# Kernel optimization log

Hardware: AMD Instinct MI355X
Metric: run time of the kernel (lower is better)

## Reference

```python
import jax, jax.numpy as jnp
import numpy as np

B, S, DIM, H = 2, 2048, 1024, 16
DK = DIM // H  # 64
NEG = -10000000000.0


def setup_inputs() -> dict:
    key = jax.random.key(0)
    k1, k2, k3, k4, k5, k6 = jax.random.split(key, 6)
    dec_xs = jax.random.normal(k1, (B, S, DIM), dtype=jnp.float32)
    enc_xs = jax.random.normal(k2, (B, S, DIM), dtype=jnp.float32)
    mask = jax.random.randint(k3, (B, S, S), 0, 2, dtype=jnp.int32)
    # torch Linear weights: out = x @ W.T, bias=False
    sc = 1.0 / np.sqrt(DIM)
    Wq = jax.random.normal(k4, (DIM, DIM), dtype=jnp.float32) * sc
    Wkv = jax.random.normal(k5, (2 * DIM, DIM), dtype=jnp.float32) * sc
    Wo = jax.random.normal(k6, (DIM, DIM), dtype=jnp.float32) * sc
    return {"dec_xs": dec_xs, "enc_xs": enc_xs, "Wq": Wq, "Wkv": Wkv, "Wo": Wo, "mask": mask}


def reference(dec_xs, enc_xs, Wq, Wkv, Wo, mask):
    b, s, dim = enc_xs.shape
    qs = dec_xs @ Wq.T                      # [b,s,dim]  (dropout inactive in eval)
    kv = enc_xs @ Wkv.T                     # [b,s,2*dim]
    ks, vs = jnp.split(kv, 2, axis=-1)
    # head layout: view(b, s, dk, h) -- heads LAST, as in the original
    qs = qs.reshape(b, s, DK, H)
    ks = ks.reshape(b, s, DK, H)
    vs = vs.reshape(b, s, DK, H)
    scores = jnp.einsum('bqdh,bkdh->bqkh', qs, ks) / np.sqrt(DK)
    scores = jnp.where(mask[..., None] == 0, NEG, scores)
    weights = jax.nn.softmax(scores, axis=-2)  # softmax over key axis
    out = jnp.einsum('bqkh,bkdh->bqdh', weights, vs).reshape(b, s, dim)
    return out @ Wo.T
```

## Files before the change

### kernel.cpp

```cpp
#include <hip/hip_runtime.h>
#include <hip/hip_bf16.h>

#define BB 2
#define SS 2048
#define DIMM 1024
#define HH 16
#define DKK 64
#define QSCALE 0.18033688011112042592f

using bf16 = __hip_bfloat16;
typedef __attribute__((ext_vector_type(8))) short v8s;
typedef __attribute__((ext_vector_type(4))) short v4s;
typedef __attribute__((ext_vector_type(4))) float f32x4;

__device__ __forceinline__ void cvt4(const float* __restrict__ s,
                                     bf16* __restrict__ d, int idx) {
  const float4 f = ((const float4*)s)[idx];
  bf16 t[4] = {__float2bfloat16(f.x), __float2bfloat16(f.y),
               __float2bfloat16(f.z), __float2bfloat16(f.w)};
  *(v4s*)(d + (size_t)idx * 4) = *(const v4s*)t;
}

__global__ __launch_bounds__(256) void convert_pack_kernel(
    const float* __restrict__ enc, const float* __restrict__ Wkv,
    const float* __restrict__ Wo, const int* __restrict__ mask,
    bf16* __restrict__ encb, bf16* __restrict__ Wkvb, bf16* __restrict__ Wob,
    unsigned long long* __restrict__ mp) {
  const int gid = blockIdx.x * 256 + threadIdx.x;
  const int NT = 256 * 1024;
#pragma unroll
  for (int i = 0; i < 4; ++i) cvt4(enc, encb, gid + i * NT);
#pragma unroll
  for (int i = 0; i < 2; ++i) cvt4(Wkv, Wkvb, gid + i * NT);
  cvt4(Wo, Wob, gid);
  const int lane = threadIdx.x & 63;
  const int wave_id = gid >> 6;
  for (int i = 0; i < 32; ++i) {
    const size_t w = (size_t)wave_id * 32 + i;
    const unsigned long long bm = __ballot(mask[w * 64 + lane] != 0);
    if (lane == 0) mp[w] = bm;
  }
}

template <bool ISQ>
__device__ __forceinline__ void proj_body(
    int t, int m0, int h0, bool isV, const float* __restrict__ dec,
    const bf16* __restrict__ encb, const float* __restrict__ Wq,
    const bf16* __restrict__ Wkvb, bf16 (*__restrict__ As)[72],
    bf16 (*__restrict__ Bs)[72], f32x4 (&acc)[4][2], int wm, int wn, int quad,
    int l15) {
  const int sr = t >> 2;
  const int sc = (t & 3) * 16;
  const int worig = (isV ? DIMM : 0) + sr * 16 + h0;

  float4 aqf[8], bqf[4];
  v8s akb[4], bkb[2];

  auto loadA = [&](int kc) {
    if (ISQ) {
#pragma unroll
      for (int rr = 0; rr < 2; ++rr) {
        const float* p = dec + (size_t)(m0 + sr + rr * 64) * DIMM + kc + sc;
#pragma unroll
        for (int i = 0; i < 4; ++i) aqf[rr * 4 + i] = ((const float4*)p)[i];
      }
    } else {
#pragma unroll
      for (int rr = 0; rr < 2; ++rr) {
        const bf16* p = encb + (size_t)(m0 + sr + rr * 64) * DIMM + kc + sc;
#pragma unroll
        for (int i = 0; i < 2; ++i) akb[rr * 2 + i] = ((const v8s*)p)[i];
      }
    }
  };
  auto loadB = [&](int kc) {
    if (ISQ) {
      const float* p = Wq + (size_t)worig * DIMM + kc + sc;
#pragma unroll
      for (int i = 0; i < 4; ++i) bqf[i] = ((const float4*)p)[i];
    } else {
      const bf16* p = Wkvb + (size_t)worig * DIMM + kc + sc;
#pragma unroll
      for (int i = 0; i < 2; ++i) bkb[i] = ((const v8s*)p)[i];
    }
  };

  loadA(0);
  loadB(0);

  for (int kc = 0; kc < DIMM; kc += 64) {
    __syncthreads();
    if (ISQ) {
#pragma unroll
      for (int rr = 0; rr < 2; ++rr) {
        bf16 tmp[16];
#pragma unroll
        for (int i = 0; i < 4; ++i) {
          const float4 f = aqf[rr * 4 + i];
          tmp[i * 4 + 0] = __float2bfloat16(f.x);
          tmp[i * 4 + 1] = __float2bfloat16(f.y);
          tmp[i * 4 + 2] = __float2bfloat16(f.z);
          tmp[i * 4 + 3] = __float2bfloat16(f.w);
        }
        *(v8s*)&As[sr + rr * 64][sc] = *(const v8s*)&tmp[0];
        *(v8s*)&As[sr + rr * 64][sc + 8] = *(const v8s*)&tmp[8];
      }
      bf16 tb[16];
#pragma unroll
      for (int i = 0; i < 4; ++i) {
        const float4 f = bqf[i];
        tb[i * 4 + 0] = __float2bfloat16(f.x);
        tb[i * 4 + 1] = __float2bfloat16(f.y);
        tb[i * 4 + 2] = __float2bfloat16(f.z);
        tb[i * 4 + 3] = __float2bfloat16(f.w);
      }
      *(v8s*)&Bs[sr][sc] = *(const v8s*)&tb[0];
      *(v8s*)&Bs[sr][sc + 8] = *(const v8s*)&tb[8];
    } else {
#pragma unroll
      for (int rr = 0; rr < 2; ++rr) {
        *(v8s*)&As[sr + rr * 64][sc] = akb[rr * 2 + 0];
        *(v8s*)&As[sr + rr * 64][sc + 8] = akb[rr * 2 + 1];
      }
      *(v8s*)&Bs[sr][sc] = bkb[0];
      *(v8s*)&Bs[sr][sc + 8] = bkb[1];
    }
    if (kc + 64 < DIMM) {
      loadA(kc + 64);
      loadB(kc + 64);
    }
    __syncthreads();
#pragma unroll
    for (int ks = 0; ks < 2; ++ks) {
      v8s af[4], bfr[2];
#pragma unroll
      for (int i = 0; i < 4; ++i)
        af[i] = *(const v8s*)&As[wm + i * 16 + l15][ks * 32 + quad * 8];
#pragma unroll
      for (int j = 0; j < 2; ++j)
        bfr[j] = *(const v8s*)&Bs[wn + j * 16 + l15][ks * 32 + quad * 8];
#pragma unroll
      for (int i = 0; i < 4; ++i)
#pragma unroll
        for (int j = 0; j < 2; ++j)
          acc[i][j] = __builtin_amdgcn_mfma_f32_16x16x32_bf16(
              af[i], bfr[j], acc[i][j], 0, 0, 0);
    }
  }
}

__global__ __launch_bounds__(256) void proj_gemm_kernel(
    const float* __restrict__ dec, const bf16* __restrict__ encb,
    const float* __restrict__ Wq, const bf16* __restrict__ Wkvb,
    bf16* __restrict__ Qr, bf16* __restrict__ Kr, bf16* __restrict__ Vt) {
  __shared__ __align__(16) bf16 As[128][72];
  __shared__ __align__(16) bf16 Bs[64][72];
  const int t = threadIdx.x;
  const int wave = t >> 6, lane = t & 63;
  const int quad = lane >> 4, l15 = lane & 15;
  const int wm = (wave >> 1) * 64, wn = (wave & 1) * 32;
  const int bx = blockIdx.x;
  const int m0 = blockIdx.y * 128;
  const bool isQ = bx < 16;
  const int kvx = bx - 16;
  const int h0 = isQ ? bx : (kvx & 15);
  const bool isV = !isQ && (kvx >= 16);

  f32x4 acc[4][2] = {};
  if (isQ)
    proj_body<true>(t, m0, h0, false, dec, encb, Wq, Wkvb, As, Bs, acc, wm, wn,
                    quad, l15);
  else
    proj_body<false>(t, m0, h0, isV, dec, encb, Wq, Wkvb, As, Bs, acc, wm, wn,
                     quad, l15);

#pragma unroll
  for (int i = 0; i < 4; ++i) {
#pragma unroll
    for (int r = 0; r < 4; ++r) {
      const int m = m0 + wm + i * 16 + quad * 4 + r;
#pragma unroll
      for (int j = 0; j < 2; ++j) {
        const int d = wn + j * 16 + l15;
        const float v = acc[i][j][r];
        if (isQ) {
          Qr[(size_t)m * DIMM + h0 * 64 + d] = __float2bfloat16(v * QSCALE);
        } else if (!isV) {
          Kr[(size_t)m * DIMM + h0 * 64 + d] = __float2bfloat16(v);
        } else {
          const int b = m >> 11, s = m & (SS - 1);
          Vt[(((size_t)b * HH + h0) * DKK + d) * SS + s] = __float2bfloat16(v);
        }
      }
    }
  }
}

__global__ __launch_bounds__(256) void out_gemm_kernel(
    const bf16* __restrict__ A, const bf16* __restrict__ W,
    float* __restrict__ out) {
  __shared__ __align__(16) bf16 As[128][72];
  __shared__ __align__(16) bf16 Bs[64][72];
  const int t = threadIdx.x;
  const int wave = t >> 6, lane = t & 63;
  const int quad = lane >> 4, l15 = lane & 15;
  const int wm = (wave >> 1) * 64, wn = (wave & 1) * 32;
  const int n0 = blockIdx.x * 64;
  const int m0 = blockIdx.y * 128;
  const int sr = t >> 2;
  const int sc = (t & 3) * 16;

  v8s ar[4], br[2];
  auto loadA = [&](int kc) {
#pragma unroll
    for (int rr = 0; rr < 2; ++rr) {
      const bf16* p = A + (size_t)(m0 + sr + rr * 64) * DIMM + kc + sc;
#pragma unroll
      for (int i = 0; i < 2; ++i) ar[rr * 2 + i] = ((const v8s*)p)[i];
    }
  };
  auto loadB = [&](int kc) {
    const bf16* p = W + (size_t)(n0 + sr) * DIMM + kc + sc;
#pragma unroll
    for (int i = 0; i < 2; ++i) br[i] = ((const v8s*)p)[i];
  };

  f32x4 acc[4][2] = {};
  loadA(0);
  loadB(0);
  for (int kc = 0; kc < DIMM; kc += 64) {
    __syncthreads();
#pragma unroll
    for (int rr = 0; rr < 2; ++rr) {
      *(v8s*)&As[sr + rr * 64][sc] = ar[rr * 2 + 0];
      *(v8s*)&As[sr + rr * 64][sc + 8] = ar[rr * 2 + 1];
    }
    *(v8s*)&Bs[sr][sc] = br[0];
    *(v8s*)&Bs[sr][sc + 8] = br[1];
    if (kc + 64 < DIMM) {
      loadA(kc + 64);
      loadB(kc + 64);
    }
    __syncthreads();
#pragma unroll
    for (int ks = 0; ks < 2; ++ks) {
      v8s af[4], bfr[2];
#pragma unroll
      for (int i = 0; i < 4; ++i)
        af[i] = *(const v8s*)&As[wm + i * 16 + l15][ks * 32 + quad * 8];
#pragma unroll
      for (int j = 0; j < 2; ++j)
        bfr[j] = *(const v8s*)&Bs[wn + j * 16 + l15][ks * 32 + quad * 8];
#pragma unroll
      for (int i = 0; i < 4; ++i)
#pragma unroll
        for (int j = 0; j < 2; ++j)
          acc[i][j] = __builtin_amdgcn_mfma_f32_16x16x32_bf16(
              af[i], bfr[j], acc[i][j], 0, 0, 0);
    }
  }

#pragma unroll
  for (int i = 0; i < 4; ++i) {
#pragma unroll
    for (int r = 0; r < 4; ++r) {
      const int m = m0 + wm + i * 16 + quad * 4 + r;
#pragma unroll
      for (int j = 0; j < 2; ++j) {
        const int n = n0 + wn + j * 16 + l15;
        out[(size_t)m * DIMM + n] = acc[i][j][r];
      }
    }
  }
}

__global__ __launch_bounds__(256) void attn_kernel(
    const bf16* __restrict__ Qr, const bf16* __restrict__ Kr,
    const bf16* __restrict__ Vt, const unsigned long long* __restrict__ mp,
    bf16* __restrict__ Ar) {
  __shared__ __align__(16) bf16 Ks[64][72];
  __shared__ __align__(16) bf16 Vs[64][72];
  __shared__ __align__(16) bf16 Ps[4][16][72];

  const int t = threadIdx.x;
  const int wave = t >> 6, lane = t & 63;
  const int quad = lane >> 4, l15 = lane & 15;

  const int bx = blockIdx.x;
  const int xcd = bx & 7, j = bx >> 3;
  const int g = (xcd << 2) | (j & 3);
  const int tile = j >> 2;
  const int h = g & 15, b = g >> 4;

  const int qw = tile * 64 + wave * 16;
  const size_t bhv = ((size_t)b * HH + h) * DKK;

  const bf16* qrow = Qr + ((size_t)(b * SS + qw + l15)) * DIMM + h * 64;
  const v8s aq0 = *(const v8s*)(qrow + quad * 8);
  const v8s aq1 = *(const v8s*)(qrow + 32 + quad * 8);

  f32x4 o[4] = {};
  float lsum[4] = {0.f, 0.f, 0.f, 0.f};

  const int id0 = t * 8;
  const int r0 = id0 >> 6, c0 = id0 & 63;

  for (int kt = 0; kt < 32; ++kt) {
    const int k0 = kt * 64;
    __syncthreads();
    {
      const bf16* kb = Kr + ((size_t)(b * SS + k0 + r0)) * DIMM + h * 64 + c0;
      *(v8s*)&Ks[r0][c0] = *(const v8s*)kb;
      *(v8s*)&Ks[r0 + 32][c0] = *(const v8s*)(kb + (size_t)32 * DIMM);
      *(v8s*)&Vs[r0][c0] = *(const v8s*)(Vt + (bhv + r0) * SS + k0 + c0);
      *(v8s*)&Vs[r0 + 32][c0] =
          *(const v8s*)(Vt + (bhv + r0 + 32) * SS + k0 + c0);
    }
    __syncthreads();

    f32x4 sc[4];
#pragma unroll
    for (int n = 0; n < 4; ++n) {
      const v8s bk0 = *(const v8s*)&Ks[n * 16 + l15][quad * 8];
      const v8s bk1 = *(const v8s*)&Ks[n * 16 + l15][32 + quad * 8];
      f32x4 z = {0.f, 0.f, 0.f, 0.f};
      z = __builtin_amdgcn_mfma_f32_16x16x32_bf16(aq0, bk0, z, 0, 0, 0);
      sc[n] = __builtin_amdgcn_mfma_f32_16x16x32_bf16(aq1, bk1, z, 0, 0, 0);
    }

    unsigned long long mw[4];
#pragma unroll
    for (int r = 0; r < 4; ++r)
      mw[r] = mp[((size_t)b * SS + qw + quad * 4 + r) * 32 + kt];
#pragma unroll
    for (int n = 0; n < 4; ++n)
#pragma unroll
      for (int r = 0; r < 4; ++r) {
        const bool keep = (mw[r] >> (n * 16 + l15)) & 1ULL;
        const float p = keep ? __builtin_amdgcn_exp2f(sc[n][r]) : 0.f;
        sc[n][r] = p;
        lsum[r] += p;
      }

#pragma unroll
    for (int n = 0; n < 4; ++n)
#pragma unroll
      for (int r = 0; r < 4; ++r)
        Ps[wave][quad * 4 + r][n * 16 + l15] = __float2bfloat16(sc[n][r]);
    const v8s ap0 = *(const v8s*)&Ps[wave][l15][quad * 8];
    const v8s ap1 = *(const v8s*)&Ps[wave][l15][32 + quad * 8];

#pragma unroll
    for (int n = 0; n < 4; ++n) {
      const v8s bv0 = *(const v8s*)&Vs[n * 16 + l15][quad * 8];
      const v8s bv1 = *(const v8s*)&Vs[n * 16 + l15][32 + quad * 8];
      o[n] = __builtin_amdgcn_mfma_f32_16x16x32_bf16(ap0, bv0, o[n], 0, 0, 0);
      o[n] = __builtin_amdgcn_mfma_f32_16x16x32_bf16(ap1, bv1, o[n], 0, 0, 0);
    }
  }

#pragma unroll
  for (int r = 0; r < 4; ++r) {
    float l = lsum[r];
    l += __shfl_xor(l, 1);
    l += __shfl_xor(l, 2);
    l += __shfl_xor(l, 4);
    l += __shfl_xor(l, 8);
    const float inv = 1.f / l;
    const size_t row = (size_t)b * SS + qw + quad * 4 + r;
#pragma unroll
    for (int n = 0; n < 4; ++n) {
      const int d = n * 16 + l15;
      Ar[row * DIMM + d * 16 + h] = __float2bfloat16(o[n][r] * inv);
    }
  }
}

extern "C" void kernel_launch(void* const* d_in, const int* in_sizes, int n_in,
                              void* d_out, int out_size, void* d_ws,
                              size_t ws_size, hipStream_t stream) {
  const float* dec = (const float*)d_in[0];
  const float* enc = (const float*)d_in[1];
  const float* Wq = (const float*)d_in[2];
  const float* Wkv = (const float*)d_in[3];
  const float* Wo = (const float*)d_in[4];
  const int* mask = (const int*)d_in[5];
  float* out = (float*)d_out;

  char* ws = (char*)d_ws;
  size_t off = 0;
  bf16* encb = (bf16*)(ws + off);
  bf16* Ar = (bf16*)(ws + off);  off += (size_t)2 * SS * DIMM * 2;
  bf16* Wkvb = (bf16*)(ws + off); off += (size_t)2 * DIMM * DIMM * 2;
  bf16* Wob = (bf16*)(ws + off);  off += (size_t)DIMM * DIMM * 2;
  bf16* Qr = (bf16*)(ws + off);   off += (size_t)2 * SS * DIMM * 2;
  bf16* Kr = (bf16*)(ws + off);   off += (size_t)2 * SS * DIMM * 2;
  bf16* Vt = (bf16*)(ws + off);   off += (size_t)2 * SS * DIMM * 2;
  unsigned long long* mp = (unsigned long long*)(ws + off);

  dim3 blk(256);
  convert_pack_kernel<<<dim3(1024), blk, 0, stream>>>(enc, Wkv, Wo, mask, encb,
                                                      Wkvb, Wob, mp);
  proj_gemm_kernel<<<dim3(48, 32), blk, 0, stream>>>(dec, encb, Wq, Wkvb, Qr,
                                                     Kr, Vt);
  attn_kernel<<<dim3(1024), blk, 0, stream>>>(Qr, Kr, Vt, mp, Ar);
  out_gemm_kernel<<<dim3(16, 32), blk, 0, stream>>>(Ar, Wob, out);
}
```

Measured before the change: 292.4 us.

## Pre-convert dec and Wq to bf16, widen projection tiles to 128x128

The decoder input and Wq are now converted to bf16 in the pack kernel, with the output buffer used as scratch, so the projection GEMM no longer converts fp32 inside its main loop. The projection tile grows from 128x64 to 128x128, each wave computing a 64x64 sub-tile. Each block covers two interleaved heads' weight rows (g*2, g*2+1) and remaps output columns accordingly. The grid shrinks from 48x32 to 24x32 blocks. In the attention kernel the mask-word load is hoisted ahead of the QK MFMAs and pre-shifted by the lane index. The trade-offs are extra conversion traffic, more registers per thread and fewer blocks in the projection.

```diff
diff --git a/kernel.cpp b/kernel.cpp
--- a/kernel.cpp
+++ b/kernel.cpp
@@ -22,14 +22,19 @@
 }
 
 __global__ __launch_bounds__(256) void convert_pack_kernel(
-    const float* __restrict__ enc, const float* __restrict__ Wkv,
+    const float* __restrict__ dec, const float* __restrict__ enc,
+    const float* __restrict__ Wq, const float* __restrict__ Wkv,
     const float* __restrict__ Wo, const int* __restrict__ mask,
-    bf16* __restrict__ encb, bf16* __restrict__ Wkvb, bf16* __restrict__ Wob,
+    bf16* __restrict__ decb, bf16* __restrict__ encb, bf16* __restrict__ Wqb,
+    bf16* __restrict__ Wkvb, bf16* __restrict__ Wob,
     unsigned long long* __restrict__ mp) {
   const int gid = blockIdx.x * 256 + threadIdx.x;
   const int NT = 256 * 1024;
 #pragma unroll
+  for (int i = 0; i < 4; ++i) cvt4(dec, decb, gid + i * NT);
+#pragma unroll
   for (int i = 0; i < 4; ++i) cvt4(enc, encb, gid + i * NT);
+  cvt4(Wq, Wqb, gid);
 #pragma unroll
   for (int i = 0; i < 2; ++i) cvt4(Wkv, Wkvb, gid + i * NT);
   cvt4(Wo, Wob, gid);
@@ -42,89 +47,61 @@
   }
 }
 
-template <bool ISQ>
-__device__ __forceinline__ void proj_body(
-    int t, int m0, int h0, bool isV, const float* __restrict__ dec,
-    const bf16* __restrict__ encb, const float* __restrict__ Wq,
-    const bf16* __restrict__ Wkvb, bf16 (*__restrict__ As)[72],
-    bf16 (*__restrict__ Bs)[72], f32x4 (&acc)[4][2], int wm, int wn, int quad,
-    int l15) {
+__global__ __launch_bounds__(256) void proj_gemm_kernel(
+    const bf16* __restrict__ decb, const bf16* __restrict__ encb,
+    const bf16* __restrict__ Wqb, const bf16* __restrict__ Wkvb,
+    bf16* __restrict__ Qr, bf16* __restrict__ Kr, bf16* __restrict__ Vt) {
+  __shared__ __align__(16) bf16 As[128][72];
+  __shared__ __align__(16) bf16 Bs[128][72];
+  const int t = threadIdx.x;
+  const int wave = t >> 6, lane = t & 63;
+  const int quad = lane >> 4, l15 = lane & 15;
+  const int wm = (wave >> 1) * 64, wn = (wave & 1) * 64;
+  const int bx = blockIdx.x;
+  const int kind = bx >> 3;
+  const int g = bx & 7;
+  const int m0 = blockIdx.y * 128;
+
+  const bf16* Asrc = (kind == 0) ? decb : encb;
+  const bf16* Wsrc = (kind == 0) ? Wqb : Wkvb;
+
   const int sr = t >> 2;
   const int sc = (t & 3) * 16;
-  const int worig = (isV ? DIMM : 0) + sr * 16 + h0;
-
-  float4 aqf[8], bqf[4];
-  v8s akb[4], bkb[2];
-
+  const int wr0 = sr * 16 + g * 2 + ((kind == 2) ? DIMM : 0);
+  const int wr1 = sr * 16 + g * 2 + 1 + ((kind == 2) ? DIMM : 0);
+
+  v8s apf[4], bpf[4];
   auto loadA = [&](int kc) {
-    if (ISQ) {
-#pragma unroll
-      for (int rr = 0; rr < 2; ++rr) {
-        const float* p = dec + (size_t)(m0 + sr + rr * 64) * DIMM + kc + sc;
-#pragma unroll
-        for (int i = 0; i < 4; ++i) aqf[rr * 4 + i] = ((const float4*)p)[i];
-      }
-    } else {
-#pragma unroll
-      for (int rr = 0; rr < 2; ++rr) {
-        const bf16* p = encb + (size_t)(m0 + sr + rr * 64) * DIMM + kc + sc;
-#pragma unroll
-        for (int i = 0; i < 2; ++i) akb[rr * 2 + i] = ((const v8s*)p)[i];
-      }
-    }
+    const bf16* p0 = Asrc + (size_t)(m0 + sr) * DIMM + kc + sc;
+    apf[0] = ((const v8s*)p0)[0];
+    apf[1] = ((const v8s*)p0)[1];
+    const bf16* p1 = Asrc + (size_t)(m0 + sr + 64) * DIMM + kc + sc;
+    apf[2] = ((const v8s*)p1)[0];
+    apf[3] = ((const v8s*)p1)[1];
   };
   auto loadB = [&](int kc) {
-    if (ISQ) {
-      const float* p = Wq + (size_t)worig * DIMM + kc + sc;
-#pragma unroll
-      for (int i = 0; i < 4; ++i) bqf[i] = ((const float4*)p)[i];
-    } else {
-      const bf16* p = Wkvb + (size_t)worig * DIMM + kc + sc;
-#pragma unroll
-      for (int i = 0; i < 2; ++i) bkb[i] = ((const v8s*)p)[i];
-    }
+    const bf16* q0 = Wsrc + (size_t)wr0 * DIMM + kc + sc;
+    bpf[0] = ((const v8s*)q0)[0];
+    bpf[1] = ((const v8s*)q0)[1];
+    const bf16* q1 = Wsrc + (size_t)wr1 * DIMM + kc + sc;
+    bpf[2] = ((const v8s*)q1)[0];
+    bpf[3] = ((const v8s*)q1)[1];
   };
 
+  f32x4 acc[4][4] = {};
   loadA(0);
   loadB(0);
 
   for (int kc = 0; kc < DIMM; kc += 64) {
     __syncthreads();
-    if (ISQ) {
-#pragma unroll
-      for (int rr = 0; rr < 2; ++rr) {
-        bf16 tmp[16];
-#pragma unroll
-        for (int i = 0; i < 4; ++i) {
-          const float4 f = aqf[rr * 4 + i];
-          tmp[i * 4 + 0] = __float2bfloat16(f.x);
-          tmp[i * 4 + 1] = __float2bfloat16(f.y);
-          tmp[i * 4 + 2] = __float2bfloat16(f.z);
-          tmp[i * 4 + 3] = __float2bfloat16(f.w);
-        }
-        *(v8s*)&As[sr + rr * 64][sc] = *(const v8s*)&tmp[0];
-        *(v8s*)&As[sr + rr * 64][sc + 8] = *(const v8s*)&tmp[8];
-      }
-      bf16 tb[16];
-#pragma unroll
-      for (int i = 0; i < 4; ++i) {
-        const float4 f = bqf[i];
-        tb[i * 4 + 0] = __float2bfloat16(f.x);
-        tb[i * 4 + 1] = __float2bfloat16(f.y);
-        tb[i * 4 + 2] = __float2bfloat16(f.z);
-        tb[i * 4 + 3] = __float2bfloat16(f.w);
-      }
-      *(v8s*)&Bs[sr][sc] = *(const v8s*)&tb[0];
-      *(v8s*)&Bs[sr][sc + 8] = *(const v8s*)&tb[8];
-    } else {
-#pragma unroll
-      for (int rr = 0; rr < 2; ++rr) {
-        *(v8s*)&As[sr + rr * 64][sc] = akb[rr * 2 + 0];
-        *(v8s*)&As[sr + rr * 64][sc + 8] = akb[rr * 2 + 1];
-      }
-      *(v8s*)&Bs[sr][sc] = bkb[0];
-      *(v8s*)&Bs[sr][sc + 8] = bkb[1];
-    }
+    *(v8s*)&As[sr][sc] = apf[0];
+    *(v8s*)&As[sr][sc + 8] = apf[1];
+    *(v8s*)&As[sr + 64][sc] = apf[2];
+    *(v8s*)&As[sr + 64][sc + 8] = apf[3];
+    *(v8s*)&Bs[sr][sc] = bpf[0];
+    *(v8s*)&Bs[sr][sc + 8] = bpf[1];
+    *(v8s*)&Bs[sr + 64][sc] = bpf[2];
+    *(v8s*)&Bs[sr + 64][sc + 8] = bpf[3];
     if (kc + 64 < DIMM) {
       loadA(kc + 64);
       loadB(kc + 64);
@@ -132,47 +109,21 @@
     __syncthreads();
 #pragma unroll
     for (int ks = 0; ks < 2; ++ks) {
-      v8s af[4], bfr[2];
+      v8s af[4], bfr[4];
 #pragma unroll
       for (int i = 0; i < 4; ++i)
         af[i] = *(const v8s*)&As[wm + i * 16 + l15][ks * 32 + quad * 8];
 #pragma unroll
-      for (int j = 0; j < 2; ++j)
+      for (int j = 0; j < 4; ++j)
         bfr[j] = *(const v8s*)&Bs[wn + j * 16 + l15][ks * 32 + quad * 8];
 #pragma unroll
       for (int i = 0; i < 4; ++i)
 #pragma unroll
-        for (int j = 0; j < 2; ++j)
+        for (int j = 0; j < 4; ++j)
           acc[i][j] = __builtin_amdgcn_mfma_f32_16x16x32_bf16(
               af[i], bfr[j], acc[i][j], 0, 0, 0);
     }
   }
-}
-
-__global__ __launch_bounds__(256) void proj_gemm_kernel(
-    const float* __restrict__ dec, const bf16* __restrict__ encb,
-    const float* __restrict__ Wq, const bf16* __restrict__ Wkvb,
-    bf16* __restrict__ Qr, bf16* __restrict__ Kr, bf16* __restrict__ Vt) {
-  __shared__ __align__(16) bf16 As[128][72];
-  __shared__ __align__(16) bf16 Bs[64][72];
-  const int t = threadIdx.x;
-  const int wave = t >> 6, lane = t & 63;
-  const int quad = lane >> 4, l15 = lane & 15;
-  const int wm = (wave >> 1) * 64, wn = (wave & 1) * 32;
-  const int bx = blockIdx.x;
-  const int m0 = blockIdx.y * 128;
-  const bool isQ = bx < 16;
-  const int kvx = bx - 16;
-  const int h0 = isQ ? bx : (kvx & 15);
-  const bool isV = !isQ && (kvx >= 16);
-
-  f32x4 acc[4][2] = {};
-  if (isQ)
-    proj_body<true>(t, m0, h0, false, dec, encb, Wq, Wkvb, As, Bs, acc, wm, wn,
-                    quad, l15);
-  else
-    proj_body<false>(t, m0, h0, isV, dec, encb, Wq, Wkvb, As, Bs, acc, wm, wn,
-                     quad, l15);
 
 #pragma unroll
   for (int i = 0; i < 4; ++i) {
@@ -180,16 +131,18 @@
     for (int r = 0; r < 4; ++r) {
       const int m = m0 + wm + i * 16 + quad * 4 + r;
 #pragma unroll
-      for (int j = 0; j < 2; ++j) {
-        const int d = wn + j * 16 + l15;
+      for (int j = 0; j < 4; ++j) {
+        const int c = wn + j * 16 + l15;
+        const int np = g * 128 + c;
         const float v = acc[i][j][r];
-        if (isQ) {
-          Qr[(size_t)m * DIMM + h0 * 64 + d] = __float2bfloat16(v * QSCALE);
-        } else if (!isV) {
-          Kr[(size_t)m * DIMM + h0 * 64 + d] = __float2bfloat16(v);
+        if (kind == 0) {
+          Qr[(size_t)m * DIMM + np] = __float2bfloat16(v * QSCALE);
+        } else if (kind == 1) {
+          Kr[(size_t)m * DIMM + np] = __float2bfloat16(v);
         } else {
+          const int h = np >> 6, d = np & 63;
           const int b = m >> 11, s = m & (SS - 1);
-          Vt[(((size_t)b * HH + h0) * DKK + d) * SS + s] = __float2bfloat16(v);
+          Vt[(((size_t)b * HH + h) * DKK + d) * SS + s] = __float2bfloat16(v);
         }
       }
     }
@@ -318,6 +271,11 @@
     }
     __syncthreads();
 
+    unsigned long long mw[4];
+#pragma unroll
+    for (int r = 0; r < 4; ++r)
+      mw[r] = mp[((size_t)b * SS + qw + quad * 4 + r) * 32 + kt] >> l15;
+
     f32x4 sc[4];
 #pragma unroll
     for (int n = 0; n < 4; ++n) {
@@ -328,15 +286,11 @@
       sc[n] = __builtin_amdgcn_mfma_f32_16x16x32_bf16(aq1, bk1, z, 0, 0, 0);
     }
 
-    unsigned long long mw[4];
-#pragma unroll
-    for (int r = 0; r < 4; ++r)
-      mw[r] = mp[((size_t)b * SS + qw + quad * 4 + r) * 32 + kt];
 #pragma unroll
     for (int n = 0; n < 4; ++n)
 #pragma unroll
       for (int r = 0; r < 4; ++r) {
-        const bool keep = (mw[r] >> (n * 16 + l15)) & 1ULL;
+        const bool keep = (mw[r] >> (n * 16)) & 1ULL;
         const float p = keep ? __builtin_amdgcn_exp2f(sc[n][r]) : 0.f;
         sc[n][r] = p;
         lsum[r] += p;
@@ -387,10 +341,13 @@
   const int* mask = (const int*)d_in[5];
   float* out = (float*)d_out;
 
+  bf16* decb = (bf16*)d_out;
+  bf16* Wqb = (bf16*)((char*)d_out + ((size_t)2 * SS * DIMM * 2));
+
   char* ws = (char*)d_ws;
   size_t off = 0;
   bf16* encb = (bf16*)(ws + off);
-  bf16* Ar = (bf16*)(ws + off);  off += (size_t)2 * SS * DIMM * 2;
+  bf16* Ar = (bf16*)(ws + off);   off += (size_t)2 * SS * DIMM * 2;
   bf16* Wkvb = (bf16*)(ws + off); off += (size_t)2 * DIMM * DIMM * 2;
   bf16* Wob = (bf16*)(ws + off);  off += (size_t)DIMM * DIMM * 2;
   bf16* Qr = (bf16*)(ws + off);   off += (size_t)2 * SS * DIMM * 2;
@@ -399,9 +356,9 @@
   unsigned long long* mp = (unsigned long long*)(ws + off);
 
   dim3 blk(256);
-  convert_pack_kernel<<<dim3(1024), blk, 0, stream>>>(enc, Wkv, Wo, mask, encb,
-                                                      Wkvb, Wob, mp);
-  proj_gemm_kernel<<<dim3(48, 32), blk, 0, stream>>>(dec, encb, Wq, Wkvb, Qr,
+  convert_pack_kernel<<<dim3(1024), blk, 0, stream>>>(
+      dec, enc, Wq, Wkv, Wo, mask, decb, encb, Wqb, Wkvb, Wob, mp);
+  proj_gemm_kernel<<<dim3(24, 32), blk, 0, stream>>>(decb, encb, Wqb, Wkvb, Qr,
                                                      Kr, Vt);
   attn_kernel<<<dim3(1024), blk, 0, stream>>>(Qr, Kr, Vt, mp, Ar);
   out_gemm_kernel<<<dim3(16, 32), blk, 0, stream>>>(Ar, Wob, out);
```

Result: no change. 286.8 us (-1.9%).
